# Kernel tuning notes

Hardware: AMD Instinct MI355X
Metric: run time of the kernel (lower is better)

Reference implementation:

```python
import jax, jax.numpy as jnp
import numpy as np

HEADS = 8
HEAD_DIM = 64
IN_DIM = HEADS * HEAD_DIM  # 512
SCALE = HEAD_DIM ** (-0.5)


def _split_heads(t):
    # [b, n, h*d] -> [b, h, n, d]
    b, n, _ = t.shape
    return t.reshape(b, n, HEADS, HEAD_DIM).transpose(0, 2, 1, 3)


def _merge_heads(t):
    # [b, h, n, d] -> [b, n, h*d]
    b, h, n, d = t.shape
    return t.transpose(0, 2, 1, 3).reshape(b, n, h * d)


def setup_inputs() -> dict:
    key = jax.random.key(0)
    ks = jax.random.split(key, 6)
    b, n = 8, 1024
    nv = jax.random.normal(ks[0], (b, n, IN_DIM), dtype=jnp.float32)
    rv = jax.random.normal(ks[1], (b, n, IN_DIM), dtype=jnp.float32)
    s = IN_DIM ** (-0.5)
    W_noise = jax.random.normal(ks[2], (IN_DIM, 2 * IN_DIM), dtype=jnp.float32) * s
    b_noise = jnp.zeros((2 * IN_DIM,), dtype=jnp.float32)
    W_rgb = jax.random.normal(ks[3], (IN_DIM, 2 * IN_DIM), dtype=jnp.float32) * s
    b_rgb = jnp.zeros((2 * IN_DIM,), dtype=jnp.float32)
    return {"nv": nv, "rv": rv, "W_noise": W_noise, "b_noise": b_noise,
            "W_rgb": W_rgb, "b_rgb": b_rgb}


def reference(nv, rv, W_noise, b_noise, W_rgb, b_rgb):
    # qk projections, chunk(2, dim=-1)
    nqk = nv @ W_noise + b_noise                      # [b, n, 2*in_dim]
    noise_q, noise_k = jnp.split(nqk, 2, axis=-1)
    rqk = rv @ W_rgb + b_rgb
    rgb_q, rgb_k = jnp.split(rqk, 2, axis=-1)

    noise_q, noise_k = _split_heads(noise_q), _split_heads(noise_k)  # [b,h,n,d]
    rgb_q, rgb_k = _split_heads(rgb_q), _split_heads(rgb_k)

    attn1 = jnp.einsum('bhnd,bhmd->bhnm', noise_q, rgb_k) * SCALE
    attn2 = jnp.einsum('bhnd,bhmd->bhnm', rgb_q, noise_k) * SCALE

    # NOTE: original uses nn.Softmax(dim=1) => softmax over the HEADS axis.
    attn1 = jax.nn.softmax(attn1, axis=1)
    attn2 = jax.nn.softmax(attn2, axis=1)

    rv_h = _split_heads(rv)  # values are the raw inputs, not projections
    nv_h = _split_heads(nv)

    noise = jnp.einsum('bhnm,bhmd->bhnd', attn1, rv_h)
    rgb = jnp.einsum('bhnm,bhmd->bhnd', attn2, nv_h)

    return (_merge_heads(noise), _merge_heads(rgb))
```

## Files before the change

kernel.cpp:

```cpp
#include <hip/hip_runtime.h>
#include <hip/hip_bf16.h>

typedef __attribute__((ext_vector_type(8))) short short8;
typedef __attribute__((ext_vector_type(4))) short short4v;
typedef __attribute__((ext_vector_type(4))) float float4v;

#define MFMA16(a, b, c) __builtin_amdgcn_mfma_f32_16x16x32_bf16(a, b, c, 0, 0, 0)

__device__ __forceinline__ short f2bf(float f) {
    __hip_bfloat16 hb = __float2bfloat16(f);
    return *reinterpret_cast<short*>(&hb);
}

__global__ __launch_bounds__(256) void wt_kernel(
    const float* __restrict__ Wn, const float* __restrict__ Wr,
    __hip_bfloat16* __restrict__ Wtn, __hip_bfloat16* __restrict__ Wtr)
{
    const int c0 = blockIdx.x * 64;
    const int k0 = blockIdx.y * 64;
    const int g  = blockIdx.z;
    const float* W = g ? Wr : Wn;
    __hip_bfloat16* Wt = g ? Wtr : Wtn;

    __shared__ short lds[64][72];
    const int t = threadIdx.x;
    {
        const int i  = t >> 2;
        const int j0 = (t & 3) * 16;
        const float* p = W + (size_t)(k0 + i) * 1024 + c0 + j0;
        #pragma unroll
        for (int jj = 0; jj < 16; ++jj)
            lds[j0 + jj][i] = f2bf(p[jj]);
    }
    __syncthreads();
    {
        const int j  = t >> 2;
        const int i0 = (t & 3) * 16;
        __hip_bfloat16* q = Wt + (size_t)(c0 + j) * 512 + k0 + i0;
        short8 v0 = *reinterpret_cast<const short8*>(&lds[j][i0]);
        short8 v1 = *reinterpret_cast<const short8*>(&lds[j][i0 + 8]);
        *reinterpret_cast<short8*>(q)     = v0;
        *reinterpret_cast<short8*>(q + 8) = v1;
    }
}

__global__ __launch_bounds__(256) void prep_kernel(
    const float* __restrict__ nv, const float* __restrict__ rv,
    __hip_bfloat16* __restrict__ Vtn, __hip_bfloat16* __restrict__ Vtr,
    __hip_bfloat16* __restrict__ An,  __hip_bfloat16* __restrict__ Ar)
{
    const int ntile = blockIdx.x & 15;
    const int src   = blockIdx.x >> 4;
    const int h     = blockIdx.y;
    const int b     = blockIdx.z;
    const float* V  = src ? rv : nv;
    __hip_bfloat16* Vt = src ? Vtr : Vtn;
    __hip_bfloat16* Ab = src ? Ar  : An;

    __shared__ short lds[64][72];
    const int t  = threadIdx.x;
    const int n0 = ntile * 64;
    {
        const int i  = t >> 2;
        const int j0 = (t & 3) * 16;
        const float* p = V + ((size_t)(b * 1024) + n0 + i) * 512 + h * 64 + j0;
        short8 a0, a1;
        #pragma unroll
        for (int jj = 0; jj < 8; ++jj) {
            short x = f2bf(p[jj]);
            a0[jj] = x; lds[j0 + jj][i] = x;
        }
        #pragma unroll
        for (int jj = 0; jj < 8; ++jj) {
            short x = f2bf(p[8 + jj]);
            a1[jj] = x; lds[j0 + 8 + jj][i] = x;
        }
        __hip_bfloat16* adst = Ab + ((size_t)(b * 1024) + n0 + i) * 512 + h * 64 + j0;
        *reinterpret_cast<short8*>(adst)     = a0;
        *reinterpret_cast<short8*>(adst + 8) = a1;
    }
    __syncthreads();
    {
        const int j  = t >> 2;
        const int i0 = (t & 3) * 16;
        __hip_bfloat16* q = Vt + (((size_t)(b * 8 + h) * 64) + j) * 1024 + n0 + i0;
        short8 v0 = *reinterpret_cast<const short8*>(&lds[j][i0]);
        short8 v1 = *reinterpret_cast<const short8*>(&lds[j][i0 + 8]);
        *reinterpret_cast<short8*>(q)     = v0;
        *reinterpret_cast<short8*>(q + 8) = v1;
    }
}

__global__ __launch_bounds__(256, 4) void proj_kernel(
    const __hip_bfloat16* __restrict__ An, const __hip_bfloat16* __restrict__ Ar,
    const __hip_bfloat16* __restrict__ Wtn, const __hip_bfloat16* __restrict__ Wtr,
    const float* __restrict__ bn, const float* __restrict__ br,
    __hip_bfloat16* __restrict__ Qn, __hip_bfloat16* __restrict__ Kn,
    __hip_bfloat16* __restrict__ Qr, __hip_bfloat16* __restrict__ Kr)
{
    const int m0 = blockIdx.x * 64;
    const int c0 = blockIdx.y * 128;
    const int g  = blockIdx.z;
    const __hip_bfloat16* A  = g ? Ar  : An;
    const __hip_bfloat16* Wt = g ? Wtr : Wtn;
    const float* bias = g ? br : bn;
    __hip_bfloat16* Qd = g ? Qr : Qn;
    __hip_bfloat16* Kd = g ? Kr : Kn;

    __shared__ short Bt[2][4][128][8];

    const int t    = threadIdx.x;
    const int lane = t & 63;
    const int w    = t >> 6;
    const int l15  = lane & 15;
    const int lg   = lane >> 4;

    auto stage = [&](int buf, int kk) {
        #pragma unroll
        for (int rep = 0; rep < 2; ++rep) {
            const int u = rep * 256 + t;
            const int s = u >> 7;
            const int c = u & 127;
            const __hip_bfloat16* src = Wt + (size_t)(c0 + c) * 512 + kk + s * 8;
            __builtin_amdgcn_global_load_lds(
                (const __attribute__((address_space(1))) unsigned int*)src,
                (__attribute__((address_space(3))) unsigned int*)&Bt[buf][s][c][0],
                16, 0, 0);
        }
    };

    float4v acc[8] = {};
    const int mrow = m0 + w * 16 + l15;

    stage(0, 0);
    __syncthreads();

    for (int kk = 0; kk < 512; kk += 32) {
        const int buf = (kk >> 5) & 1;
        if (kk < 480) stage(buf ^ 1, kk + 32);
        short8 afrag = *reinterpret_cast<const short8*>(
            A + (size_t)mrow * 512 + kk + lg * 8);
        #pragma unroll
        for (int cs = 0; cs < 8; ++cs) {
            short8 bfrag = *reinterpret_cast<const short8*>(
                &Bt[buf][lg][cs * 16 + l15][0]);
            acc[cs] = MFMA16(afrag, bfrag, acc[cs]);
        }
        __syncthreads();
    }

    #pragma unroll
    for (int cs = 0; cs < 8; ++cs) {
        const int c  = c0 + cs * 16 + l15;
        const bool isK = (c >= 512);
        const int hh = (c >> 6) & 7;
        const int d  = c & 63;
        __hip_bfloat16* dst = isK ? Kd : Qd;
        const float bv = bias[c];
        #pragma unroll
        for (int r = 0; r < 4; ++r) {
            const int m = m0 + w * 16 + lg * 4 + r;
            const int b = m >> 10, n = m & 1023;
            dst[(((size_t)(b * 8 + hh) * 1024 + n) * 64) + d] =
                __float2bfloat16(acc[cs][r] + bv);
        }
    }
}

__global__ __launch_bounds__(512, 2) void attn_kernel(
    const __hip_bfloat16* __restrict__ Qn, const __hip_bfloat16* __restrict__ Kn,
    const __hip_bfloat16* __restrict__ Qr, const __hip_bfloat16* __restrict__ Kr,
    const __hip_bfloat16* __restrict__ Vtn, const __hip_bfloat16* __restrict__ Vtr,
    float* __restrict__ out)
{
    const int combo = blockIdx.x;
    const int bb    = combo & 7;
    const int dir   = combo >> 3;
    const int nt    = blockIdx.y;
    const __hip_bfloat16* Q  = dir ? Qr  : Qn;
    const __hip_bfloat16* K  = dir ? Kn  : Kr;
    const __hip_bfloat16* Vt = dir ? Vtn : Vtr;
    float* O = out + (size_t)dir * (8u * 1024u * 512u);

    const int t    = threadIdx.x;
    const int lane = t & 63;
    const int w    = t >> 6;
    const int iw   = w & 1;
    const int hg   = w >> 1;
    const int h0   = hg * 2;
    const int l15  = lane & 15;
    const int lg   = lane >> 4;

    __shared__ short K_s[2][8 * 32 * 64];
    __shared__ short P_s[8][32][40];
    __shared__ float X_s[2][2][4][2][512];

    const int n0 = nt * 64;
    const float C = 0.125f * 1.44269504f;

    const __hip_bfloat16* Vb[2] = {
        Vt + (size_t)((bb * 8 + h0)     * 64) * 1024,
        Vt + (size_t)((bb * 8 + h0 + 1) * 64) * 1024 };

    auto stage = [&](int bufn, int mt) {
        #pragma unroll
        for (int i = 0; i < 4; ++i) {
            const int u    = (w * 4 + i) * 64 + lane;
            const int h    = u >> 8;
            const int mr   = (u >> 3) & 31;
            const int slot = (u & 7) ^ (mr & 7);
            const __hip_bfloat16* g =
                K + ((size_t)((bb * 8 + h) * 1024) + mt + mr) * 64 + slot * 8;
            __builtin_amdgcn_global_load_lds(
                (const __attribute__((address_space(1))) unsigned int*)g,
                (__attribute__((address_space(3))) unsigned int*)&K_s[bufn][u * 8],
                16, 0, 0);
        }
    };

    short8 qf[2][2][2];
    #pragma unroll
    for (int ns = 0; ns < 2; ++ns)
        #pragma unroll
        for (int hh = 0; hh < 2; ++hh)
            #pragma unroll
            for (int kc = 0; kc < 2; ++kc)
                qf[ns][hh][kc] = *reinterpret_cast<const short8*>(
                    Q + ((size_t)((bb * 8 + h0 + hh) * 1024) + n0 + ns * 32 + iw * 16 + l15) * 64
                      + kc * 32 + lg * 8);

    float4v oacc[2][2][4] = {};

    stage(0, 0);
    __syncthreads();

    for (int it = 0; it < 32; ++it) {
        const int m0  = it << 5;
        const int buf = it & 1;
        const int par = it & 1;
        stage(buf ^ 1, (it < 31) ? m0 + 32 : 0);
        short8 vf[2][4];
        #pragma unroll
        for (int hh = 0; hh < 2; ++hh)
            #pragma unroll
            for (int dd = 0; dd < 4; ++dd)
                vf[hh][dd] = *reinterpret_cast<const short8*>(
                    Vb[hh] + (size_t)(dd * 16 + l15) * 1024 + m0 + lg * 8);
        short8 kf[2][2][2];
        const short* ks = K_s[buf];
        #pragma unroll
        for (int hh = 0; hh < 2; ++hh)
            #pragma unroll
            for (int j = 0; j < 2; ++j) {
                const int mr = j * 16 + l15;
                #pragma unroll
                for (int kc = 0; kc < 2; ++kc)
                    kf[hh][j][kc] = *reinterpret_cast<const short8*>(
                        ks + (h0 + hh) * 2048 + mr * 64
                           + (((kc * 4 + lg) ^ (mr & 7)) * 8));
            }
        float e[2][2][8];
        float ps[2][8];
        #pragma unroll
        for (int ns = 0; ns < 2; ++ns) {
            float4v sacc[2][2] = {};
            #pragma unroll
            for (int hh = 0; hh < 2; ++hh)
                #pragma unroll
                for (int j = 0; j < 2; ++j)
                    #pragma unroll
                    for (int kc = 0; kc < 2; ++kc)
                        sacc[hh][j] = MFMA16(kf[hh][j][kc], qf[ns][hh][kc], sacc[hh][j]);
            #pragma unroll
            for (int p = 0; p < 8; ++p) ps[ns][p] = 0.f;
            #pragma unroll
            for (int hh = 0; hh < 2; ++hh)
                #pragma unroll
                for (int j = 0; j < 2; ++j)
                    #pragma unroll
                    for (int r = 0; r < 4; ++r) {
                        float ev = exp2f(sacc[hh][j][r] * C);
                        e[ns][hh][j * 4 + r] = ev;
                        ps[ns][j * 4 + r] += ev;
                    }
            #pragma unroll
            for (int p = 0; p < 8; ++p)
                X_s[par][ns][hg][iw][p * 64 + lane] = ps[ns][p];
        }
        __syncthreads();
        #pragma unroll
        for (int ns = 0; ns < 2; ++ns) {
            float inv[8];
            #pragma unroll
            for (int p = 0; p < 8; ++p) {
                float tot = ps[ns][p];
                #pragma unroll
                for (int g = 1; g < 4; ++g)
                    tot += X_s[par][ns][(hg + g) & 3][iw][p * 64 + lane];
                inv[p] = __builtin_amdgcn_rcpf(tot);
            }
            #pragma unroll
            for (int hh = 0; hh < 2; ++hh)
                #pragma unroll
                for (int j = 0; j < 2; ++j) {
                    short4v pk;
                    #pragma unroll
                    for (int r = 0; r < 4; ++r)
                        pk[r] = f2bf(e[ns][hh][j * 4 + r] * inv[j * 4 + r]);
                    *reinterpret_cast<short4v*>(
                        &P_s[h0 + hh][iw * 16 + l15][j * 16 + lg * 4]) = pk;
                }
            #pragma unroll
            for (int hh = 0; hh < 2; ++hh) {
                short8 pf = *reinterpret_cast<const short8*>(
                    &P_s[h0 + hh][iw * 16 + l15][lg * 8]);
                #pragma unroll
                for (int dd = 0; dd < 4; ++dd)
                    oacc[ns][hh][dd] = MFMA16(pf, vf[hh][dd], oacc[ns][hh][dd]);
            }
        }
    }

    #pragma unroll
    for (int ns = 0; ns < 2; ++ns)
        #pragma unroll
        for (int hh = 0; hh < 2; ++hh)
            #pragma unroll
            for (int dd = 0; dd < 4; ++dd)
                #pragma unroll
                for (int r = 0; r < 4; ++r) {
                    const int n = n0 + ns * 32 + iw * 16 + lg * 4 + r;
                    const int d = dd * 16 + l15;
                    O[((size_t)(bb * 1024) + n) * 512 + (h0 + hh) * 64 + d] =
                        oacc[ns][hh][dd][r];
                }
}

extern "C" void kernel_launch(void* const* d_in, const int* in_sizes, int n_in,
                              void* d_out, int out_size, void* d_ws, size_t ws_size,
                              hipStream_t stream) {
    const float* nv = (const float*)d_in[0];
    const float* rv = (const float*)d_in[1];
    const float* Wn = (const float*)d_in[2];
    const float* bn = (const float*)d_in[3];
    const float* Wr = (const float*)d_in[4];
    const float* br = (const float*)d_in[5];
    float* out = (float*)d_out;

    __hip_bfloat16* w = (__hip_bfloat16*)d_ws;
    const size_t E = 8ull * 8 * 1024 * 64;
    __hip_bfloat16* Qn  = w;
    __hip_bfloat16* Kn  = w + E;
    __hip_bfloat16* Qr  = w + 2 * E;
    __hip_bfloat16* Kr  = w + 3 * E;
    __hip_bfloat16* Vtn = w + 4 * E;
    __hip_bfloat16* Vtr = w + 5 * E;
    __hip_bfloat16* An  = w + 6 * E;
    __hip_bfloat16* Ar  = w + 7 * E;
    __hip_bfloat16* Wtn = w + 8 * E;
    __hip_bfloat16* Wtr = w + 8 * E + 512 * 1024;

    wt_kernel  <<<dim3(16, 8, 2), 256, 0, stream>>>(Wn, Wr, Wtn, Wtr);
    prep_kernel<<<dim3(32, 8, 8), 256, 0, stream>>>(nv, rv, Vtn, Vtr, An, Ar);
    proj_kernel<<<dim3(128, 8, 2), 256, 0, stream>>>(An, Ar, Wtn, Wtr, bn, br,
                                                     Qn, Kn, Qr, Kr);
    attn_kernel<<<dim3(16, 16), 512, 0, stream>>>(Qn, Kn, Qr, Kr, Vtn, Vtr, out);
}
```

Measured before the change: 179.3 us.

## Halve attention query tile and single-buffer K to raise occupancy

The attention kernel now processes 32 query rows per block instead of 64, doubling the grid to 512 blocks. K staging moves from double buffering to a single LDS buffer, and the softmax-sum scratch drops its parity and sub-tile dimensions, cutting LDS use and registers. Launch bounds are raised to allow more resident blocks per CU. The aim is better latency hiding through more waves, at the cost of reloading K and V twice as often and serializing the K prefetch behind a barrier.

```diff
diff --git a/kernel.cpp b/kernel.cpp
--- a/kernel.cpp
+++ b/kernel.cpp
@@ -167,7 +167,7 @@
     }
 }
 
-__global__ __launch_bounds__(512, 2) void attn_kernel(
+__global__ __launch_bounds__(512, 4) void attn_kernel(
     const __hip_bfloat16* __restrict__ Qn, const __hip_bfloat16* __restrict__ Kn,
     const __hip_bfloat16* __restrict__ Qr, const __hip_bfloat16* __restrict__ Kr,
     const __hip_bfloat16* __restrict__ Vtn, const __hip_bfloat16* __restrict__ Vtr,
@@ -191,18 +191,18 @@
     const int l15  = lane & 15;
     const int lg   = lane >> 4;
 
-    __shared__ short K_s[2][8 * 32 * 64];
+    __shared__ short K_s[8 * 32 * 64];
     __shared__ short P_s[8][32][40];
-    __shared__ float X_s[2][2][4][2][512];
-
-    const int n0 = nt * 64;
+    __shared__ float X_s[4][2][512];
+
+    const int n0 = nt * 32;
     const float C = 0.125f * 1.44269504f;
 
     const __hip_bfloat16* Vb[2] = {
         Vt + (size_t)((bb * 8 + h0)     * 64) * 1024,
         Vt + (size_t)((bb * 8 + h0 + 1) * 64) * 1024 };
 
-    auto stage = [&](int bufn, int mt) {
+    auto stage = [&](int mt) {
         #pragma unroll
         for (int i = 0; i < 4; ++i) {
             const int u    = (w * 4 + i) * 64 + lane;
@@ -213,32 +213,61 @@
                 K + ((size_t)((bb * 8 + h) * 1024) + mt + mr) * 64 + slot * 8;
             __builtin_amdgcn_global_load_lds(
                 (const __attribute__((address_space(1))) unsigned int*)g,
-                (__attribute__((address_space(3))) unsigned int*)&K_s[bufn][u * 8],
+                (__attribute__((address_space(3))) unsigned int*)&K_s[u * 8],
                 16, 0, 0);
         }
     };
 
-    short8 qf[2][2][2];
+    short8 qf[2][2];
     #pragma unroll
-    for (int ns = 0; ns < 2; ++ns)
+    for (int hh = 0; hh < 2; ++hh)
+        #pragma unroll
+        for (int kc = 0; kc < 2; ++kc)
+            qf[hh][kc] = *reinterpret_cast<const short8*>(
+                Q + ((size_t)((bb * 8 + h0 + hh) * 1024) + n0 + iw * 16 + l15) * 64
+                  + kc * 32 + lg * 8);
+
+    float4v oacc[2][4] = {};
+
+    stage(0);
+    __syncthreads();
+
+    for (int it = 0; it < 32; ++it) {
+        const int m0 = it << 5;
+        float4v sacc[2][2];
+        #pragma unroll
+        for (int hh = 0; hh < 2; ++hh) {
+            const short* ks = K_s + (h0 + hh) * 2048;
+            #pragma unroll
+            for (int j = 0; j < 2; ++j) {
+                const int mr = j * 16 + l15;
+                short8 k0 = *reinterpret_cast<const short8*>(
+                    ks + mr * 64 + ((lg ^ (mr & 7)) * 8));
+                short8 k1 = *reinterpret_cast<const short8*>(
+                    ks + mr * 64 + (((4 + lg) ^ (mr & 7)) * 8));
+                float4v s = {};
+                s = MFMA16(k0, qf[hh][0], s);
+                s = MFMA16(k1, qf[hh][1], s);
+                sacc[hh][j] = s;
+            }
+        }
+        float e[2][8];
+        float ps[8] = {0.f, 0.f, 0.f, 0.f, 0.f, 0.f, 0.f, 0.f};
         #pragma unroll
         for (int hh = 0; hh < 2; ++hh)
             #pragma unroll
-            for (int kc = 0; kc < 2; ++kc)
-                qf[ns][hh][kc] = *reinterpret_cast<const short8*>(
-                    Q + ((size_t)((bb * 8 + h0 + hh) * 1024) + n0 + ns * 32 + iw * 16 + l15) * 64
-                      + kc * 32 + lg * 8);
-
-    float4v oacc[2][2][4] = {};
-
-    stage(0, 0);
-    __syncthreads();
-
-    for (int it = 0; it < 32; ++it) {
-        const int m0  = it << 5;
-        const int buf = it & 1;
-        const int par = it & 1;
-        stage(buf ^ 1, (it < 31) ? m0 + 32 : 0);
+            for (int j = 0; j < 2; ++j)
+                #pragma unroll
+                for (int r = 0; r < 4; ++r) {
+                    float ev = exp2f(sacc[hh][j][r] * C);
+                    e[hh][j * 4 + r] = ev;
+                    ps[j * 4 + r] += ev;
+                }
+        #pragma unroll
+        for (int p = 0; p < 8; ++p)
+            X_s[hg][iw][p * 64 + lane] = ps[p];
+        __syncthreads();
+        if (it < 31) stage(m0 + 32);
         short8 vf[2][4];
         #pragma unroll
         for (int hh = 0; hh < 2; ++hh)
@@ -246,94 +275,48 @@
             for (int dd = 0; dd < 4; ++dd)
                 vf[hh][dd] = *reinterpret_cast<const short8*>(
                     Vb[hh] + (size_t)(dd * 16 + l15) * 1024 + m0 + lg * 8);
-        short8 kf[2][2][2];
-        const short* ks = K_s[buf];
+        float inv[8];
+        #pragma unroll
+        for (int p = 0; p < 8; ++p) {
+            float tot = ps[p];
+            #pragma unroll
+            for (int g = 1; g < 4; ++g)
+                tot += X_s[(hg + g) & 3][iw][p * 64 + lane];
+            inv[p] = __builtin_amdgcn_rcpf(tot);
+        }
         #pragma unroll
         for (int hh = 0; hh < 2; ++hh)
             #pragma unroll
             for (int j = 0; j < 2; ++j) {
-                const int mr = j * 16 + l15;
+                short4v pk;
                 #pragma unroll
-                for (int kc = 0; kc < 2; ++kc)
-                    kf[hh][j][kc] = *reinterpret_cast<const short8*>(
-                        ks + (h0 + hh) * 2048 + mr * 64
-                           + (((kc * 4 + lg) ^ (mr & 7)) * 8));
+                for (int r = 0; r < 4; ++r)
+                    pk[r] = f2bf(e[hh][j * 4 + r] * inv[j * 4 + r]);
+                *reinterpret_cast<short4v*>(
+                    &P_s[h0 + hh][iw * 16 + l15][j * 16 + lg * 4]) = pk;
             }
-        float e[2][2][8];
-        float ps[2][8];
-        #pragma unroll
-        for (int ns = 0; ns < 2; ++ns) {
-            float4v sacc[2][2] = {};
-            #pragma unroll
-            for (int hh = 0; hh < 2; ++hh)
-                #pragma unroll
-                for (int j = 0; j < 2; ++j)
-                    #pragma unroll
-                    for (int kc = 0; kc < 2; ++kc)
-                        sacc[hh][j] = MFMA16(kf[hh][j][kc], qf[ns][hh][kc], sacc[hh][j]);
-            #pragma unroll
-            for (int p = 0; p < 8; ++p) ps[ns][p] = 0.f;
-            #pragma unroll
-            for (int hh = 0; hh < 2; ++hh)
-                #pragma unroll
-                for (int j = 0; j < 2; ++j)
-                    #pragma unroll
-                    for (int r = 0; r < 4; ++r) {
-                        float ev = exp2f(sacc[hh][j][r] * C);
-                        e[ns][hh][j * 4 + r] = ev;
-                        ps[ns][j * 4 + r] += ev;
-                    }
-            #pragma unroll
-            for (int p = 0; p < 8; ++p)
-                X_s[par][ns][hg][iw][p * 64 + lane] = ps[ns][p];
+        #pragma unroll
+        for (int hh = 0; hh < 2; ++hh) {
+            short8 pf = *reinterpret_cast<const short8*>(
+                &P_s[h0 + hh][iw * 16 + l15][lg * 8]);
+            #pragma unroll
+            for (int dd = 0; dd < 4; ++dd)
+                oacc[hh][dd] = MFMA16(pf, vf[hh][dd], oacc[hh][dd]);
         }
         __syncthreads();
-        #pragma unroll
-        for (int ns = 0; ns < 2; ++ns) {
-            float inv[8];
-            #pragma unroll
-            for (int p = 0; p < 8; ++p) {
-                float tot = ps[ns][p];
-                #pragma unroll
-                for (int g = 1; g < 4; ++g)
-                    tot += X_s[par][ns][(hg + g) & 3][iw][p * 64 + lane];
-                inv[p] = __builtin_amdgcn_rcpf(tot);
+    }
+
+    #pragma unroll
+    for (int hh = 0; hh < 2; ++hh)
+        #pragma unroll
+        for (int dd = 0; dd < 4; ++dd)
+            #pragma unroll
+            for (int r = 0; r < 4; ++r) {
+                const int n = n0 + iw * 16 + lg * 4 + r;
+                const int d = dd * 16 + l15;
+                O[((size_t)(bb * 1024) + n) * 512 + (h0 + hh) * 64 + d] =
+                    oacc[hh][dd][r];
             }
-            #pragma unroll
-            for (int hh = 0; hh < 2; ++hh)
-                #pragma unroll
-                for (int j = 0; j < 2; ++j) {
-                    short4v pk;
-                    #pragma unroll
-                    for (int r = 0; r < 4; ++r)
-                        pk[r] = f2bf(e[ns][hh][j * 4 + r] * inv[j * 4 + r]);
-                    *reinterpret_cast<short4v*>(
-                        &P_s[h0 + hh][iw * 16 + l15][j * 16 + lg * 4]) = pk;
-                }
-            #pragma unroll
-            for (int hh = 0; hh < 2; ++hh) {
-                short8 pf = *reinterpret_cast<const short8*>(
-                    &P_s[h0 + hh][iw * 16 + l15][lg * 8]);
-                #pragma unroll
-                for (int dd = 0; dd < 4; ++dd)
-                    oacc[ns][hh][dd] = MFMA16(pf, vf[hh][dd], oacc[ns][hh][dd]);
-            }
-        }
-    }
-
-    #pragma unroll
-    for (int ns = 0; ns < 2; ++ns)
-        #pragma unroll
-        for (int hh = 0; hh < 2; ++hh)
-            #pragma unroll
-            for (int dd = 0; dd < 4; ++dd)
-                #pragma unroll
-                for (int r = 0; r < 4; ++r) {
-                    const int n = n0 + ns * 32 + iw * 16 + lg * 4 + r;
-                    const int d = dd * 16 + l15;
-                    O[((size_t)(bb * 1024) + n) * 512 + (h0 + hh) * 64 + d] =
-                        oacc[ns][hh][dd][r];
-                }
 }
 
 extern "C" void kernel_launch(void* const* d_in, const int* in_sizes, int n_in,
@@ -364,5 +347,5 @@
     prep_kernel<<<dim3(32, 8, 8), 256, 0, stream>>>(nv, rv, Vtn, Vtr, An, Ar);
     proj_kernel<<<dim3(128, 8, 2), 256, 0, stream>>>(An, Ar, Wtn, Wtr, bn, br,
                                                      Qn, Kn, Qr, Kr);
-    attn_kernel<<<dim3(16, 16), 512, 0, stream>>>(Qn, Kn, Qr, Kr, Vtn, Vtr, out);
-}
+    attn_kernel<<<dim3(16, 32), 512, 0, stream>>>(Qn, Kn, Qr, Kr, Vtn, Vtr, out);
+}
```

After: 225.7 us. 1.26x slower.
